# Kernel tuning notes

Measured on AMD Instinct MI355X. Metric: run time of the kernel, lower is better.

## Reference

```python
import jax, jax.numpy as jnp
import numpy as np

EMBED_DIM = 64
GAMMA = 1.0
N_X = 8192
N_Y = 8192


def _self_attention(inputs, W_q, W_k):
    # inputs: [n, d]; W_q, W_k: [d, d]
    q = inputs @ W_q
    k = inputs @ W_k
    scores = jax.nn.softmax(q @ k.T / jnp.sqrt(jnp.float32(EMBED_DIM)), axis=-1)  # [n, n]
    return scores @ inputs  # [n, d]


def setup_inputs() -> dict:
    key = jax.random.key(0)
    k1, k2, k3, k4 = jax.random.split(key, 4)
    return {
        "rotation_params": jax.random.normal(k1, (EMBED_DIM, EMBED_DIM), dtype=jnp.float32),
        "entangle_params": jax.random.normal(k2, (EMBED_DIM, EMBED_DIM), dtype=jnp.float32),
        "x": jax.random.normal(k3, (N_X, EMBED_DIM), dtype=jnp.float32),
        "y": jax.random.normal(k4, (N_Y, EMBED_DIM), dtype=jnp.float32),
    }


def reference(rotation_params, entangle_params, x, y):
    x_att = _self_attention(x, rotation_params, entangle_params)  # [n_x, d]
    y_att = _self_attention(y, rotation_params, entangle_params)  # [n_y, d]
    # Pairwise squared distances, vectorizing the original per-pair loop.
    diff = x_att[:, None, :] - y_att[None, :, :]  # [n_x, n_y, d]
    sq = jnp.sum(diff * diff, axis=-1)  # [n_x, n_y]
    return jnp.exp(-GAMMA * sq)
```

## Files before the change

### kernel.cpp

```cpp
#include <hip/hip_runtime.h>
#include <math.h>

#define N 8192
#define D 64
#define KS 4
#define LOG2E 1.4426950408889634f

typedef _Float16 half_t;
typedef _Float16 f16x8 __attribute__((ext_vector_type(8)));
typedef _Float16 f16x4 __attribute__((ext_vector_type(4)));
typedef float f32x4 __attribute__((ext_vector_type(4)));

#define MFMA32(a, b, c) __builtin_amdgcn_mfma_f32_16x16x32_f16((a), (b), (c), 0, 0, 0)

#define SPLIT(v, H, L) { half_t _h = (half_t)(v); (H) = _h; (L) = (half_t)((v) - (float)_h); }


__global__ __launch_bounds__(256) void proj_kernel(
    const float* __restrict__ Wq, const float* __restrict__ Wk,
    const float* __restrict__ X, const float* __restrict__ Y,
    half_t* __restrict__ Qfx, half_t* __restrict__ Qfy,
    half_t* __restrict__ Kfx, half_t* __restrict__ Kfy)
{
    __shared__ float sWq[64][64];
    __shared__ float sWk[64][64];
    __shared__ float sIn[16][64];
    const int t = threadIdx.x;
#pragma unroll
    for (int p = 0; p < 16; ++p) {
        int idx = p * 256 + t;
        sWq[idx >> 6][idx & 63] = Wq[idx];
        sWk[idx >> 6][idx & 63] = Wk[idx];
    }
    const int R0 = blockIdx.x * 16;
    const float* src; half_t* dqf; half_t* dkf; int r0;
    if (R0 < N) { src = X; dqf = Qfx; dkf = Kfx; r0 = R0; }
    else        { src = Y; dqf = Qfy; dkf = Kfy; r0 = R0 - N; }
#pragma unroll
    for (int p = 0; p < 4; ++p) {
        int idx = p * 256 + t;
        sIn[idx >> 6][idx & 63] = src[(size_t)r0 * D + idx];
    }
    __syncthreads();
    const int c = t & 63;
    const int rb = t >> 6;
    const int ksi = c >> 5, quadi = (c >> 3) & 3, j = c & 7;
#pragma unroll
    for (int rr = 0; rr < 4; ++rr) {
        int r = rr * 4 + rb;
        float aq = 0.f, ak = 0.f;
#pragma unroll
        for (int k = 0; k < 64; ++k) {
            float xv = sIn[r][k];
            aq = fmaf(xv, sWq[k][c], aq);
            ak = fmaf(xv, sWk[k][c], ak);
        }
        aq *= (0.125f * LOG2E);
        int rg = r0 + r;
        int tile = rg >> 5, tau = (rg >> 4) & 1, c16l = rg & 15;
        size_t idx = (size_t)tile * 4096 + ksi * 2048 + tau * 1024
                   + (quadi * 16 + c16l) * 8 + j;
        half_t qhh = (half_t)aq;
        dqf[idx]       = qhh;
        dqf[idx + 512] = (half_t)(aq - (float)qhh);
        half_t khh = (half_t)ak;
        dkf[idx]       = khh;
        dkf[idx + 512] = (half_t)(ak - (float)khh);
    }
}

__global__ __launch_bounds__(256) void ztprep_kernel(
    const float* __restrict__ X, const float* __restrict__ Y,
    half_t* __restrict__ Zfx, half_t* __restrict__ Zfy)
{
    const int t = threadIdx.x;
    const int tile = blockIdx.x;
    const float* src = blockIdx.y ? Y : X;
    half_t* dst = blockIdx.y ? Zfy : Zfx;
    const int dt = t >> 6, lane = t & 63;
    const int quad = lane >> 4, c16 = lane & 15;
    f16x8 h;
#pragma unroll
    for (int j = 0; j < 8; ++j)
        h[j] = (half_t)src[(size_t)(tile * 32 + quad * 8 + j) * D + dt * 16 + c16];
    *(f16x8*)&dst[(size_t)tile * 2048 + dt * 512 + lane * 8] = h;
}

__global__ __launch_bounds__(256, 2) void attn_kernel(
    const half_t* __restrict__ Qfx, const half_t* __restrict__ Qfy,
    const half_t* __restrict__ Kfx, const half_t* __restrict__ Kfy,
    const half_t* __restrict__ Zfx, const half_t* __restrict__ Zfy,
    half_t* __restrict__ Opart, float* __restrict__ mpart, float* __restrict__ lpart)
{
    const int side = blockIdx.y;
    const half_t* Qf = side ? Qfy : Qfx;
    const half_t* Kf = side ? Kfy : Kfx;
    const half_t* Zf = side ? Zfy : Zfx;
    const int t = threadIdx.x, w = t >> 6, lane = t & 63;
    const int c16 = lane & 15, quad = lane >> 4;
    const int q0 = blockIdx.x * 128 + w * 32;
    const int tile0 = blockIdx.z * (N / KS / 32);
    const int ITERS = (N / KS) / 32;

    __shared__ half_t Pbuf[4][32][40];
    half_t (*Phi)[40] = Pbuf[w];

    f16x8 qh[2][2], ql[2][2];
    {
        const half_t* qb = Qf + (size_t)(q0 >> 5) * 4096 + lane * 8;
#pragma unroll
        for (int ks = 0; ks < 2; ++ks)
#pragma unroll
            for (int qg = 0; qg < 2; ++qg) {
                qh[qg][ks] = *(const f16x8*)&qb[ks * 2048 + qg * 1024];
                ql[qg][ks] = *(const f16x8*)&qb[ks * 2048 + qg * 1024 + 512];
            }
    }

    f32x4 ot[4][2] = {};
    f32x4 lacc[2] = {};
    float m_run[2] = {-INFINITY, -INFINITY};
    f16x8 ones;
#pragma unroll
    for (int i = 0; i < 8; ++i) ones[i] = (half_t)1.0f;

    f16x8 kAh[2][2], kAl[2][2], kBh[2][2], kBl[2][2];
    f32x4 stA[2][2], stB[2][2];

    auto loadK = [&](int tile, f16x8 (&kh)[2][2], f16x8 (&kl)[2][2]) {
        const half_t* b = Kf + (size_t)tile * 4096 + lane * 8;
#pragma unroll
        for (int ks = 0; ks < 2; ++ks)
#pragma unroll
            for (int tau = 0; tau < 2; ++tau) {
                kh[ks][tau] = *(const f16x8*)&b[ks * 2048 + tau * 1024];
                kl[ks][tau] = *(const f16x8*)&b[ks * 2048 + tau * 1024 + 512];
            }
    };
    auto doS = [&](f32x4 (&st)[2][2], f16x8 (&kh)[2][2], f16x8 (&kl)[2][2]) {
        const f32x4 zero = {};
#pragma unroll
        for (int qg = 0; qg < 2; ++qg)
#pragma unroll
            for (int tau = 0; tau < 2; ++tau) st[qg][tau] = zero;
#pragma unroll
        for (int ks = 0; ks < 2; ++ks)
#pragma unroll
            for (int tau = 0; tau < 2; ++tau)
#pragma unroll
                for (int qg = 0; qg < 2; ++qg) {
                    st[qg][tau] = MFMA32(kh[ks][tau], qh[qg][ks], st[qg][tau]);
                    st[qg][tau] = MFMA32(kh[ks][tau], ql[qg][ks], st[qg][tau]);
                    st[qg][tau] = MFMA32(kl[ks][tau], qh[qg][ks], st[qg][tau]);
                }
    };

    auto body = [&](int tt, f32x4 (&stCur)[2][2], f32x4 (&stNext)[2][2],
                    f16x8 (&kNh)[2][2], f16x8 (&kNl)[2][2],
                    f16x8 (&kRh)[2][2], f16x8 (&kRl)[2][2]) {
        if (tt + 1 < ITERS) doS(stNext, kNh, kNl);
        if (tt + 2 < ITERS) loadK(tile0 + tt + 2, kRh, kRl);
        const half_t* zb = Zf + (size_t)(tile0 + tt) * 2048 + lane * 8;
        f16x8 zh[4];
#pragma unroll
        for (int dt = 0; dt < 4; ++dt)
            zh[dt] = *(const f16x8*)&zb[dt * 512];
#pragma unroll
        for (int qg = 0; qg < 2; ++qg) {
            float mt = fmaxf(fmaxf(fmaxf(stCur[qg][0][0], stCur[qg][0][1]),
                                   fmaxf(stCur[qg][0][2], stCur[qg][0][3])),
                             fmaxf(fmaxf(stCur[qg][1][0], stCur[qg][1][1]),
                                   fmaxf(stCur[qg][1][2], stCur[qg][1][3])));
            mt = fmaxf(mt, __shfl_xor(mt, 16));
            mt = fmaxf(mt, __shfl_xor(mt, 32));
            float mn = fmaxf(m_run[qg], mt);
            float al = exp2f(m_run[qg] - mn);
            m_run[qg] = mn;
#pragma unroll
            for (int tau = 0; tau < 2; ++tau) {
                f16x4 h4;
#pragma unroll
                for (int r = 0; r < 4; ++r)
                    h4[r] = (half_t)exp2f(stCur[qg][tau][r] - mn);
                *(f16x4*)&Phi[16 * qg + c16][16 * tau + 4 * quad] = h4;
            }
            lacc[qg] *= al;
#pragma unroll
            for (int dt = 0; dt < 4; ++dt) ot[dt][qg] *= al;
        }
        f16x8 pbh[2];
#pragma unroll
        for (int qg = 0; qg < 2; ++qg)
            pbh[qg] = *(const f16x8*)&Phi[16 * qg + c16][quad * 8];
#pragma unroll
        for (int dt = 0; dt < 4; ++dt)
#pragma unroll
            for (int qg = 0; qg < 2; ++qg)
                ot[dt][qg] = MFMA32(zh[dt], pbh[qg], ot[dt][qg]);
#pragma unroll
        for (int qg = 0; qg < 2; ++qg)
            lacc[qg] = MFMA32(ones, pbh[qg], lacc[qg]);
    };

    loadK(tile0, kAh, kAl);
    doS(stA, kAh, kAl);
    if (ITERS > 1) loadK(tile0 + 1, kBh, kBl);
#pragma unroll 1
    for (int tt = 0; tt < ITERS; tt += 2) {
        body(tt,     stA, stB, kBh, kBl, kAh, kAl);
        body(tt + 1, stB, stA, kAh, kAl, kBh, kBl);
    }

    const size_t obase = (size_t)(side * KS + blockIdx.z) * N;
#pragma unroll
    for (int qg = 0; qg < 2; ++qg) {
        int q = q0 + 16 * qg + c16;
#pragma unroll
        for (int dt = 0; dt < 4; ++dt) {
            f16x4 o4;
#pragma unroll
            for (int r = 0; r < 4; ++r) o4[r] = (half_t)ot[dt][qg][r];
            *(f16x4*)&Opart[(obase + q) * D + 16 * dt + 4 * quad] = o4;
        }
        if (quad == 0) {
            mpart[obase + q] = m_run[qg];
            lpart[obase + q] = lacc[qg][0];
        }
    }
}

__global__ __launch_bounds__(256) void combine_kernel(
    const half_t* __restrict__ Opart, const float* __restrict__ mpart,
    const float* __restrict__ lpart,
    half_t* __restrict__ Xf, half_t* __restrict__ Yf,
    float* __restrict__ n2x, float* __restrict__ n2y)
{
    const int side = blockIdx.y;
    const int q = blockIdx.x * 16 + (threadIdx.x >> 4);
    const int d4 = (threadIdx.x & 15) * 4;
    float m[KS], l[KS];
#pragma unroll
    for (int s = 0; s < KS; ++s) {
        size_t b = (size_t)(side * KS + s) * N + q;
        m[s] = mpart[b]; l[s] = lpart[b];
    }
    float M = -INFINITY;
#pragma unroll
    for (int s = 0; s < KS; ++s) M = fmaxf(M, m[s]);
    float L = 0.f;
    f32x4 o = {0.f, 0.f, 0.f, 0.f};
#pragma unroll
    for (int s = 0; s < KS; ++s) {
        float sc = exp2f(m[s] - M);
        L += l[s] * sc;
        f16x4 p4 = *(const f16x4*)&Opart[((size_t)(side * KS + s) * N + q) * D + d4];
#pragma unroll
        for (int i = 0; i < 4; ++i) o[i] = fmaf((float)p4[i], sc, o[i]);
    }
    const float oscale = (side ? 1.0f : 2.0f * LOG2E) / L;
    f16x4 h4;
#pragma unroll
    for (int i = 0; i < 4; ++i) h4[i] = (half_t)(o[i] * oscale);
    float sq = 0.f;
#pragma unroll
    for (int i = 0; i < 4; ++i) { float hv = (float)h4[i]; sq = fmaf(hv, hv, sq); }
#pragma unroll
    for (int off = 1; off < 16; off <<= 1) sq += __shfl_xor(sq, off);
    half_t* dst = side ? Yf : Xf;
    float*  n2  = side ? n2y : n2x;
    if ((threadIdx.x & 15) == 0)
        n2[q] = side ? sq * LOG2E : sq * (0.25f / LOG2E);
    const int tile16 = q >> 4, c16l = q & 15;
    const int ksi = d4 >> 5, quadi = (d4 >> 3) & 3, j0 = d4 & 7;
    *(f16x4*)&dst[(size_t)tile16 * 1024 + ksi * 512 + (quadi * 16 + c16l) * 8 + j0] = h4;
}

__global__ __launch_bounds__(256, 4) void rbf_kernel(
    const half_t* __restrict__ Xf, const half_t* __restrict__ Yf,
    const float* __restrict__ n2x, const float* __restrict__ n2y,
    float* __restrict__ out)
{
    const int t = threadIdx.x, w = t >> 6, lane = t & 63;
    const int c16 = lane & 15, quad = lane >> 4;
    const int X0 = blockIdx.y * 128 + (w >> 1) * 64;
    const int Y0 = blockIdx.x * 128 + (w & 1) * 64;
    float ny[4];
    f32x4 nx4[4];
#pragma unroll
    for (int yt = 0; yt < 4; ++yt) ny[yt] = n2y[Y0 + 16 * yt + c16];
#pragma unroll
    for (int xt = 0; xt < 4; ++xt)
        nx4[xt] = *(const f32x4*)&n2x[X0 + 16 * xt + 4 * quad];

    const half_t* Xb = Xf + lane * 8;
    const half_t* Yb = Yf + lane * 8;
    f32x4 acc[4][4] = {};
#pragma unroll
    for (int ks = 0; ks < 2; ++ks) {
        f16x8 bh[4];
#pragma unroll
        for (int yt = 0; yt < 4; ++yt)
            bh[yt] = *(const f16x8*)&Yb[(size_t)((Y0 >> 4) + yt) * 1024 + ks * 512];
#pragma unroll
        for (int xt = 0; xt < 4; ++xt) {
            f16x8 ah = *(const f16x8*)&Xb[(size_t)((X0 >> 4) + xt) * 1024 + ks * 512];
#pragma unroll
            for (int yt = 0; yt < 4; ++yt)
                acc[xt][yt] = MFMA32(ah, bh[yt], acc[xt][yt]);
        }
    }
#pragma unroll
    for (int xt = 0; xt < 4; ++xt)
#pragma unroll
        for (int r = 0; r < 4; ++r) {
            int xr = X0 + 16 * xt + 4 * quad + r;
            float nx = nx4[xt][r];
#pragma unroll
            for (int yt = 0; yt < 4; ++yt) {
                float v = exp2f(acc[xt][yt][r] - nx - ny[yt]);
                out[(size_t)xr * N + Y0 + 16 * yt + c16] = v;
            }
        }
}

extern "C" void kernel_launch(void* const* d_in, const int* in_sizes, int n_in,
                              void* d_out, int out_size, void* d_ws, size_t ws_size,
                              hipStream_t stream) {
    const float* Wq = (const float*)d_in[0];
    const float* Wk = (const float*)d_in[1];
    const float* x  = (const float*)d_in[2];
    const float* y  = (const float*)d_in[3];
    float* out = (float*)d_out;

    char* p = (char*)d_ws;
    size_t used = 0;
    auto alloc = [&](size_t bytes) -> void* {
        void* r = (void*)(p + used);
        used += (bytes + 255) & ~(size_t)255;
        return r;
    };
    half_t* Qfx = (half_t*)alloc((size_t)N * D * 2 * 2);
    half_t* Qfy = (half_t*)alloc((size_t)N * D * 2 * 2);
    half_t* Kfx = (half_t*)alloc((size_t)N * D * 2 * 2);
    half_t* Kfy = (half_t*)alloc((size_t)N * D * 2 * 2);
    half_t* Zfx = (half_t*)alloc((size_t)N * D * 2);
    half_t* Zfy = (half_t*)alloc((size_t)N * D * 2);
    half_t* Xf  = (half_t*)alloc((size_t)N * D * 2);
    half_t* Yf  = (half_t*)alloc((size_t)N * D * 2);
    float*  n2x = (float*) alloc((size_t)N * 4);
    float*  n2y = (float*) alloc((size_t)N * 4);
    half_t* Opart = (half_t*)alloc((size_t)2 * KS * N * D * 2);
    float*  mpart = (float*) alloc((size_t)2 * KS * N * 4);
    float*  lpart = (float*) alloc((size_t)2 * KS * N * 4);

    proj_kernel<<<dim3(2 * N / 16), 256, 0, stream>>>(Wq, Wk, x, y,
                                                      Qfx, Qfy, Kfx, Kfy);
    ztprep_kernel<<<dim3(N / 32, 2), 256, 0, stream>>>(x, y, Zfx, Zfy);
    attn_kernel<<<dim3(N / 128, 2, KS), 256, 0, stream>>>(
        Qfx, Qfy, Kfx, Kfy, Zfx, Zfy, Opart, mpart, lpart);
    combine_kernel<<<dim3(N / 16, 2), 256, 0, stream>>>(
        Opart, mpart, lpart, Xf, Yf, n2x, n2y);
    rbf_kernel<<<dim3(N / 128, N / 128), 256, 0, stream>>>(Xf, Yf, n2x, n2y, out);
}
```

Measured before the change: 390.1 us.

## Stage K/V tiles through shared memory and vectorize RBF output stores

The attention kernel now loads each K and Z tile cooperatively once per block into a triple-buffered shared-memory ring, instead of every wave loading the full tile from global memory on its own. It also raises wave priority around the MFMA blocks. The RBF kernel swaps the MFMA operand roles so each lane holds four consecutive output columns, and it writes them with 128-bit nontemporal stores instead of scalar stores. The aims are less redundant global traffic in attention and better coalesced streaming writes for the large 8192x8192 output, at the cost of two extra barriers per attention iteration and more LDS use.

```diff
diff --git a/kernel.cpp b/kernel.cpp
--- a/kernel.cpp
+++ b/kernel.cpp
@@ -102,6 +102,8 @@
     const int tile0 = blockIdx.z * (N / KS / 32);
     const int ITERS = (N / KS) / 32;
 
+    __shared__ half_t Ksh[3][4096];
+    __shared__ half_t Zsh[3][2048];
     __shared__ half_t Pbuf[4][32][40];
     half_t (*Phi)[40] = Pbuf[w];
 
@@ -124,11 +126,23 @@
 #pragma unroll
     for (int i = 0; i < 8; ++i) ones[i] = (half_t)1.0f;
 
-    f16x8 kAh[2][2], kAl[2][2], kBh[2][2], kBl[2][2];
     f32x4 stA[2][2], stB[2][2];
-
-    auto loadK = [&](int tile, f16x8 (&kh)[2][2], f16x8 (&kl)[2][2]) {
-        const half_t* b = Kf + (size_t)tile * 4096 + lane * 8;
+    f16x8 g[3];
+
+    auto stage_load = [&](int tile) {
+        const half_t* kb = Kf + (size_t)tile * 4096 + t * 8;
+        g[0] = *(const f16x8*)(kb);
+        g[1] = *(const f16x8*)(kb + 2048);
+        g[2] = *(const f16x8*)(Zf + (size_t)tile * 2048 + t * 8);
+    };
+    auto stage_write = [&](int slot) {
+        *(f16x8*)&Ksh[slot][t * 8]        = g[0];
+        *(f16x8*)&Ksh[slot][t * 8 + 2048] = g[1];
+        *(f16x8*)&Zsh[slot][t * 8]        = g[2];
+    };
+    auto doS = [&](f32x4 (&st)[2][2], int slot) {
+        f16x8 kh[2][2], kl[2][2];
+        const half_t* b = &Ksh[slot][lane * 8];
 #pragma unroll
         for (int ks = 0; ks < 2; ++ks)
 #pragma unroll
@@ -136,13 +150,12 @@
                 kh[ks][tau] = *(const f16x8*)&b[ks * 2048 + tau * 1024];
                 kl[ks][tau] = *(const f16x8*)&b[ks * 2048 + tau * 1024 + 512];
             }
-    };
-    auto doS = [&](f32x4 (&st)[2][2], f16x8 (&kh)[2][2], f16x8 (&kl)[2][2]) {
         const f32x4 zero = {};
 #pragma unroll
         for (int qg = 0; qg < 2; ++qg)
 #pragma unroll
             for (int tau = 0; tau < 2; ++tau) st[qg][tau] = zero;
+        __builtin_amdgcn_s_setprio(1);
 #pragma unroll
         for (int ks = 0; ks < 2; ++ks)
 #pragma unroll
@@ -153,14 +166,16 @@
                     st[qg][tau] = MFMA32(kh[ks][tau], ql[qg][ks], st[qg][tau]);
                     st[qg][tau] = MFMA32(kl[ks][tau], qh[qg][ks], st[qg][tau]);
                 }
-    };
-
-    auto body = [&](int tt, f32x4 (&stCur)[2][2], f32x4 (&stNext)[2][2],
-                    f16x8 (&kNh)[2][2], f16x8 (&kNl)[2][2],
-                    f16x8 (&kRh)[2][2], f16x8 (&kRl)[2][2]) {
-        if (tt + 1 < ITERS) doS(stNext, kNh, kNl);
-        if (tt + 2 < ITERS) loadK(tile0 + tt + 2, kRh, kRl);
-        const half_t* zb = Zf + (size_t)(tile0 + tt) * 2048 + lane * 8;
+        __builtin_amdgcn_s_setprio(0);
+    };
+
+    auto body = [&](int tt, f32x4 (&stCur)[2][2], f32x4 (&stNext)[2][2]) {
+        __syncthreads();
+        if (tt + 1 < ITERS) stage_write((tt + 1) % 3);
+        __syncthreads();
+        if (tt + 2 < ITERS) stage_load(tile0 + tt + 2);
+        if (tt + 1 < ITERS) doS(stNext, (tt + 1) % 3);
+        const half_t* zb = &Zsh[tt % 3][lane * 8];
         f16x8 zh[4];
 #pragma unroll
         for (int dt = 0; dt < 4; ++dt)
@@ -192,6 +207,7 @@
 #pragma unroll
         for (int qg = 0; qg < 2; ++qg)
             pbh[qg] = *(const f16x8*)&Phi[16 * qg + c16][quad * 8];
+        __builtin_amdgcn_s_setprio(1);
 #pragma unroll
         for (int dt = 0; dt < 4; ++dt)
 #pragma unroll
@@ -200,15 +216,18 @@
 #pragma unroll
         for (int qg = 0; qg < 2; ++qg)
             lacc[qg] = MFMA32(ones, pbh[qg], lacc[qg]);
-    };
-
-    loadK(tile0, kAh, kAl);
-    doS(stA, kAh, kAl);
-    if (ITERS > 1) loadK(tile0 + 1, kBh, kBl);
+        __builtin_amdgcn_s_setprio(0);
+    };
+
+    stage_load(tile0);
+    stage_write(0);
+    stage_load(tile0 + 1);
+    __syncthreads();
+    doS(stA, 0);
 #pragma unroll 1
     for (int tt = 0; tt < ITERS; tt += 2) {
-        body(tt,     stA, stB, kBh, kBl, kAh, kAl);
-        body(tt + 1, stB, stA, kAh, kAl, kBh, kBl);
+        body(tt,     stA, stB);
+        body(tt + 1, stB, stA);
     }
 
     const size_t obase = (size_t)(side * KS + blockIdx.z) * N;
@@ -284,43 +303,44 @@
     const int c16 = lane & 15, quad = lane >> 4;
     const int X0 = blockIdx.y * 128 + (w >> 1) * 64;
     const int Y0 = blockIdx.x * 128 + (w & 1) * 64;
-    float ny[4];
-    f32x4 nx4[4];
-#pragma unroll
-    for (int yt = 0; yt < 4; ++yt) ny[yt] = n2y[Y0 + 16 * yt + c16];
-#pragma unroll
-    for (int xt = 0; xt < 4; ++xt)
-        nx4[xt] = *(const f32x4*)&n2x[X0 + 16 * xt + 4 * quad];
+    float nx[4];
+    f32x4 ny4[4];
+#pragma unroll
+    for (int xt = 0; xt < 4; ++xt) nx[xt] = n2x[X0 + 16 * xt + c16];
+#pragma unroll
+    for (int yt = 0; yt < 4; ++yt)
+        ny4[yt] = *(const f32x4*)&n2y[Y0 + 16 * yt + 4 * quad];
 
     const half_t* Xb = Xf + lane * 8;
     const half_t* Yb = Yf + lane * 8;
     f32x4 acc[4][4] = {};
 #pragma unroll
     for (int ks = 0; ks < 2; ++ks) {
-        f16x8 bh[4];
-#pragma unroll
-        for (int yt = 0; yt < 4; ++yt)
-            bh[yt] = *(const f16x8*)&Yb[(size_t)((Y0 >> 4) + yt) * 1024 + ks * 512];
-#pragma unroll
-        for (int xt = 0; xt < 4; ++xt) {
-            f16x8 ah = *(const f16x8*)&Xb[(size_t)((X0 >> 4) + xt) * 1024 + ks * 512];
-#pragma unroll
-            for (int yt = 0; yt < 4; ++yt)
-                acc[xt][yt] = MFMA32(ah, bh[yt], acc[xt][yt]);
-        }
-    }
-#pragma unroll
-    for (int xt = 0; xt < 4; ++xt)
-#pragma unroll
-        for (int r = 0; r < 4; ++r) {
-            int xr = X0 + 16 * xt + 4 * quad + r;
-            float nx = nx4[xt][r];
-#pragma unroll
-            for (int yt = 0; yt < 4; ++yt) {
-                float v = exp2f(acc[xt][yt][r] - nx - ny[yt]);
-                out[(size_t)xr * N + Y0 + 16 * yt + c16] = v;
-            }
-        }
+        f16x8 ax[4];
+#pragma unroll
+        for (int xt = 0; xt < 4; ++xt)
+            ax[xt] = *(const f16x8*)&Xb[(size_t)((X0 >> 4) + xt) * 1024 + ks * 512];
+#pragma unroll
+        for (int yt = 0; yt < 4; ++yt) {
+            f16x8 ay = *(const f16x8*)&Yb[(size_t)((Y0 >> 4) + yt) * 1024 + ks * 512];
+#pragma unroll
+            for (int xt = 0; xt < 4; ++xt)
+                acc[yt][xt] = MFMA32(ay, ax[xt], acc[yt][xt]);
+        }
+    }
+#pragma unroll
+    for (int xt = 0; xt < 4; ++xt) {
+        const int xr = X0 + 16 * xt + c16;
+        float* rowp = out + (size_t)xr * N + Y0 + 4 * quad;
+#pragma unroll
+        for (int yt = 0; yt < 4; ++yt) {
+            f32x4 v;
+#pragma unroll
+            for (int r = 0; r < 4; ++r)
+                v[r] = exp2f(acc[yt][xt][r] - nx[xt] - ny4[yt][r]);
+            __builtin_nontemporal_store(v, (f32x4*)(rowp + 16 * yt));
+        }
+    }
 }
 
 extern "C" void kernel_launch(void* const* d_in, const int* in_sizes, int n_in,
```

Measured after the change: 427.8 us. +9.7%, slower.
